# Kernel tuning notes

Measured on AMD Instinct MI355X. Metric: run time of the kernel, lower is better.

The kernel has to match this reference:

```python
import jax, jax.numpy as jnp
import numpy as np

B, C_IN, H, W = 64, 2048, 14, 14
D, FF, G, NC, NH = 768, 2048, 100, 9605, 8
DF = int(NC / G + 0.999)  # 97
HD = D // NH
EPS = 1e-5


def _ln(x, g, b):
    m = jnp.mean(x, axis=-1, keepdims=True)
    v = jnp.mean(jnp.square(x - m), axis=-1, keepdims=True)
    return (x - m) * jax.lax.rsqrt(v + EPS) * g + b


def setup_inputs() -> dict:
    key = jax.random.key(0)
    ks = jax.random.split(key, 16)
    def xav(k, shape):
        fan_in, fan_out = shape[-1], shape[-2] if len(shape) > 1 else shape[-1]
        std = float(np.sqrt(2.0 / (fan_in + fan_out)))
        return jax.random.normal(k, shape, jnp.float32) * std
    return {
        "x": jax.random.normal(ks[0], (B, C_IN, H, W), jnp.float32),
        "w_embed": xav(ks[1], (D, C_IN)), "b_embed": jnp.zeros((D,), jnp.float32),
        "query_embed": jax.random.normal(ks[2], (G, D), jnp.float32),
        "wq": xav(ks[3], (D, D)), "bq": jnp.zeros((D,), jnp.float32),
        "wk": xav(ks[4], (D, D)), "bk": jnp.zeros((D,), jnp.float32),
        "wv": xav(ks[5], (D, D)), "bv": jnp.zeros((D,), jnp.float32),
        "wo": xav(ks[6], (D, D)), "bo": jnp.zeros((D,), jnp.float32),
        "g1": jnp.ones((D,), jnp.float32), "be1": jnp.zeros((D,), jnp.float32),
        "g2": jnp.ones((D,), jnp.float32), "be2": jnp.zeros((D,), jnp.float32),
        "g3": jnp.ones((D,), jnp.float32), "be3": jnp.zeros((D,), jnp.float32),
        "w1": xav(ks[7], (FF, D)), "bl1": jnp.zeros((FF,), jnp.float32),
        "w2": xav(ks[8], (D, FF)), "bl2": jnp.zeros((D,), jnp.float32),
        "dup_pool": xav(ks[9], (G, D, DF)),
        "dup_bias": jnp.zeros((NC,), jnp.float32),
    }


def reference(x, w_embed, b_embed, query_embed, wq, bq, wk, bk, wv, bv, wo, bo,
              g1, be1, g2, be2, g3, be3, w1, bl1, w2, bl2, dup_pool, dup_bias):
    bs = x.shape[0]
    # [B, C, H, W] -> [B, S, C]
    mem = x.reshape(bs, x.shape[1], -1).transpose(0, 2, 1)
    # embed_standart + relu -> [B, S, D]
    mem = jax.nn.relu(jnp.einsum('bsc,dc->bsd', mem, w_embed) + b_embed)
    # tgt = queries broadcast to batch: [B, G, D]
    tgt = jnp.broadcast_to(query_embed[None], (bs, G, D))
    # layer: tgt = norm1(tgt + dropout1(tgt)) = norm1(2*tgt)
    tgt = _ln(tgt + tgt, g1, be1)
    # cross multihead attention (q=tgt, k=v=mem)
    q = (jnp.einsum('bgd,ed->bge', tgt, wq) + bq).reshape(bs, G, NH, HD)
    k = (jnp.einsum('bsd,ed->bse', mem, wk) + bk).reshape(bs, -1, NH, HD)
    v = (jnp.einsum('bsd,ed->bse', mem, wv) + bv).reshape(bs, -1, NH, HD)
    scores = jnp.einsum('bghd,bshd->bhgs', q, k) / jnp.sqrt(jnp.float32(HD))
    attn = jax.nn.softmax(scores, axis=-1)
    ctx = jnp.einsum('bhgs,bshd->bghd', attn, v).reshape(bs, G, D)
    ctx = jnp.einsum('bgd,ed->bge', ctx, wo) + bo
    tgt = _ln(tgt + ctx, g2, be2)
    # FFN
    ff = jax.nn.relu(jnp.einsum('bgd,fd->bgf', tgt, w1) + bl1)
    ff = jnp.einsum('bgf,df->bgd', ff, w2) + bl2
    h = _ln(tgt + ff, g3, be3)  # [B, G, D]
    # grouped FC: per-group matmul fused into one batched einsum
    out_extrap = jnp.einsum('bgd,gdf->bgf', h, dup_pool)  # [B, G, DF]
    logits = out_extrap.reshape(bs, G * DF)[:, :NC] + dup_bias
    return logits
```

## Files before the change

kernel.cpp:

```cpp
#include <hip/hip_runtime.h>
#include <hip/hip_bf16.h>


#define B_    64
#define CIN_  2048
#define S_    196
#define D_    768
#define FF_   2048
#define G_    100
#define NC_   9605
#define NH_   8
#define HD_   96
#define DF_   97
#define FP_   112
#define GP_   112
#define SP_   224
#define KVW_  1536
#define BS_   (B_ * S_)
#define BG_   (B_ * G_)

typedef __bf16 bf16x8 __attribute__((ext_vector_type(8)));
typedef float  f32x4  __attribute__((ext_vector_type(4)));

__device__ __forceinline__ float bf2f(ushort u) {
  union { unsigned int i; float f; } v; v.i = ((unsigned int)u) << 16; return v.f;
}
__device__ __forceinline__ ushort f2bf(float f) {
  __hip_bfloat16 h = __float2bfloat16(f);
  return *reinterpret_cast<ushort*>(&h);
}

__device__ __forceinline__ void gl2lds16(const ushort* g, ushort* l) {
  __builtin_amdgcn_global_load_lds((const __attribute__((address_space(1))) unsigned int*)g,
                                   (__attribute__((address_space(3))) unsigned int*)l, 16, 0, 0);
}

struct CvtArgs {
  const float* src[7];
  ushort*      dst[7];
  int          n4[7];
  int          total;
};
__global__ void k_cvtall(CvtArgs a) {
  int i = blockIdx.x * blockDim.x + threadIdx.x;
  const int stride = gridDim.x * blockDim.x;
  for (; i < a.total; i += stride) {
    int seg = 0, off = i;
    while (off >= a.n4[seg]) { off -= a.n4[seg]; ++seg; }
    float4 v = ((const float4*)a.src[seg])[off];
    ushort4 o;
    o.x = f2bf(v.x); o.y = f2bf(v.y); o.z = f2bf(v.z); o.w = f2bf(v.w);
    ((ushort4*)a.dst[seg])[off] = o;
  }
}

__global__ void k_packb(const float* __restrict__ bk, const float* __restrict__ bv,
                        float* __restrict__ bkv) {
  int i = blockIdx.x * 256 + threadIdx.x;
  if (i < D_) bkv[i] = bk[i];
  else if (i < 2 * D_) bkv[i] = bv[i - D_];
}

__global__ __launch_bounds__(256) void k_xpose(const float* __restrict__ x, ushort* __restrict__ A) {
  __shared__ float tile[32][33];
  const int c0 = blockIdx.x * 32, s0 = blockIdx.y * 32, b = blockIdx.z;
  const int t = threadIdx.x;
  const int tx = t & 31, ty = t >> 5;
  const float* xb = x + (size_t)b * CIN_ * S_;
  #pragma unroll
  for (int r = 0; r < 32; r += 8) {
    int c = c0 + ty + r, s = s0 + tx;
    tile[ty + r][tx] = (s < S_) ? xb[(size_t)c * S_ + s] : 0.f;
  }
  __syncthreads();
  const int sl = t >> 3, cq = (t & 7) * 4;
  const int s = s0 + sl;
  if (s < S_) {
    ushort4 o;
    o.x = f2bf(tile[cq + 0][sl]);
    o.y = f2bf(tile[cq + 1][sl]);
    o.z = f2bf(tile[cq + 2][sl]);
    o.w = f2bf(tile[cq + 3][sl]);
    *(ushort4*)&A[((size_t)(b * S_ + s)) * CIN_ + c0 + cq] = o;
  }
}

__global__ __launch_bounds__(256) void k_dupT(const float* __restrict__ dup, ushort* __restrict__ dupT) {
  __shared__ float tile[32][33];
  const int f0 = blockIdx.x * 32, d0 = blockIdx.y * 32, g = blockIdx.z;
  const int tx = threadIdx.x & 31, ty = threadIdx.x >> 5;
  #pragma unroll
  for (int r = 0; r < 32; r += 8) {
    int d = d0 + ty + r, f = f0 + tx;
    tile[ty + r][tx] = (f < DF_) ? dup[(size_t)g * D_ * DF_ + (size_t)d * DF_ + f] : 0.f;
  }
  __syncthreads();
  #pragma unroll
  for (int r = 0; r < 32; r += 8) {
    int f = f0 + ty + r, d = d0 + tx;
    if (f < FP_) dupT[((size_t)g * FP_ + f) * D_ + d] = f2bf(tile[tx][ty + r]);
  }
}

__global__ __launch_bounds__(256) void k_vT(const ushort* __restrict__ KVb, ushort* __restrict__ VbT) {
  __shared__ ushort tile[32][33];
  const int s0 = blockIdx.x * 32, d0 = blockIdx.y * 32, bh = blockIdx.z;
  const int b = bh >> 3, h = bh & 7;
  const int tx = threadIdx.x & 31, ty = threadIdx.x >> 5;
  #pragma unroll
  for (int r = 0; r < 32; r += 8) {
    int s = s0 + ty + r, d = d0 + tx;
    tile[ty + r][tx] = (s < S_) ? KVb[((size_t)(b * S_ + s)) * KVW_ + D_ + h * HD_ + d] : (ushort)0;
  }
  __syncthreads();
  #pragma unroll
  for (int r = 0; r < 32; r += 8) {
    int d = d0 + ty + r, s = s0 + tx;
    VbT[((size_t)bh * HD_ + d) * SP_ + s] = tile[tx][ty + r];
  }
}

__global__ __launch_bounds__(256) void k_tgt(const float* __restrict__ qe,
    const float* __restrict__ g1, const float* __restrict__ be1,
    float* __restrict__ tgt, ushort* __restrict__ tgtB) {
  const int g = blockIdx.x, t = threadIdx.x;
  if (g >= G_) {
    for (int d = t; d < D_; d += 256) tgtB[(size_t)g * D_ + d] = 0;
    return;
  }
  __shared__ float r1[256], r2[256];
  float y[3]; float s = 0.f, sq = 0.f;
  const float* row = qe + (size_t)g * D_;
  #pragma unroll
  for (int i = 0; i < 3; ++i) { float v = 2.f * row[t + i * 256]; y[i] = v; s += v; sq += v * v; }
  r1[t] = s; r2[t] = sq; __syncthreads();
  for (int o = 128; o > 0; o >>= 1) { if (t < o) { r1[t] += r1[t + o]; r2[t] += r2[t + o]; } __syncthreads(); }
  const float mean = r1[0] * (1.f / D_);
  const float var  = r2[0] * (1.f / D_) - mean * mean;
  const float w = rsqrtf(var + 1e-5f);
  #pragma unroll
  for (int i = 0; i < 3; ++i) {
    int d = t + i * 256;
    float v = (y[i] - mean) * w * g1[d] + be1[d];
    tgt[(size_t)g * D_ + d] = v;
    tgtB[(size_t)g * D_ + d] = f2bf(v);
  }
}

__global__ __launch_bounds__(256) void k_gemm(const ushort* __restrict__ A, const ushort* __restrict__ B,
    const float* __restrict__ bias, float* __restrict__ Cf, ushort* __restrict__ Cb,
    int N, int K, int nbx, int nm, int relu) {
  const int l = blockIdx.x;
  const int mb = (l >> 3) / nbx * 8 + (l & 7);
  const int nb = (l >> 3) % nbx;
  if (mb >= nm) return;
  __shared__ ushort As[128 * 32];
  __shared__ ushort Bs[128 * 32];
  const int t = threadIdx.x;
  const int m0 = mb * 128, n0 = nb * 128;
  const int lane = t & 63, wave = t >> 6;
  const int quad = lane >> 4, lrow = lane & 15;
  const int wr = (wave >> 1) * 64, wc = (wave & 1) * 64;
  const int srow = t >> 2, scol = (t & 3) * 8;
  f32x4 acc[4][4] = {};
  for (int k0 = 0; k0 < K; k0 += 32) {
    const ushort* ag = A + (size_t)(m0 + srow) * K + k0 + scol;
    const ushort* bg = B + (size_t)(n0 + srow) * K + k0 + scol;
    gl2lds16(ag,                    &As[srow * 32 + scol]);
    gl2lds16(ag + (size_t)64 * K,   &As[(srow + 64) * 32 + scol]);
    gl2lds16(bg,                    &Bs[srow * 32 + scol]);
    gl2lds16(bg + (size_t)64 * K,   &Bs[(srow + 64) * 32 + scol]);
    __syncthreads();
    bf16x8 af[4], bfr[4];
    #pragma unroll
    for (int i = 0; i < 4; ++i) af[i] = *(const bf16x8*)&As[(wr + i * 16 + lrow) * 32 + quad * 8];
    #pragma unroll
    for (int j = 0; j < 4; ++j) bfr[j] = *(const bf16x8*)&Bs[(wc + j * 16 + lrow) * 32 + quad * 8];
    #pragma unroll
    for (int i = 0; i < 4; ++i)
      #pragma unroll
      for (int j = 0; j < 4; ++j)
        acc[i][j] = __builtin_amdgcn_mfma_f32_16x16x32_bf16(af[i], bfr[j], acc[i][j], 0, 0, 0);
    __syncthreads();
  }
  #pragma unroll
  for (int i = 0; i < 4; ++i) {
    #pragma unroll
    for (int j = 0; j < 4; ++j) {
      const int gcol = n0 + wc + j * 16 + lrow;
      const float bv = bias ? bias[gcol] : 0.f;
      #pragma unroll
      for (int r = 0; r < 4; ++r) {
        const int grow = m0 + wr + i * 16 + quad * 4 + r;
        float v = acc[i][j][r] + bv;
        if (relu) v = fmaxf(v, 0.f);
        if (Cf) Cf[(size_t)grow * N + gcol] = v;
        else    Cb[(size_t)grow * N + gcol] = f2bf(v);
      }
    }
  }
}
static inline int swz_grid(int nm, int nbx) { return ((nm + 7) & ~7) * nbx; }

__global__ __launch_bounds__(256) void k_scores(const ushort* __restrict__ qB,
    const ushort* __restrict__ KVb, ushort* __restrict__ attnP) {
  __shared__ ushort Ks[208 * HD_];
  const int h = blockIdx.x, b = blockIdx.y, t = threadIdx.x;
  const int bh = b * NH_ + h;
  const int lane = t & 63, wave = t >> 6;
  const int quad = lane >> 4, c = lane & 15;
  for (int i = t; i < 208 * 12; i += 256) {
    int r = i / 12, col = (i % 12) * 8;
    gl2lds16(KVb + ((size_t)(b * S_ + r)) * KVW_ + h * HD_ + col, &Ks[i * 8]);
  }
  __syncthreads();
  const float scale = 0.1020620726f;
  for (int ii = wave; ii < 7; ii += 4) {
    f32x4 acc[13] = {};
    bf16x8 af[3];
    #pragma unroll
    for (int ks = 0; ks < 3; ++ks)
      af[ks] = *(const bf16x8*)(qB + ((size_t)(ii * 16 + c)) * D_ + h * HD_ + ks * 32 + quad * 8);
    #pragma unroll
    for (int j = 0; j < 13; ++j) {
      #pragma unroll
      for (int ks = 0; ks < 3; ++ks) {
        bf16x8 bf = *(const bf16x8*)&Ks[(j * 16 + c) * HD_ + ks * 32 + quad * 8];
        acc[j] = __builtin_amdgcn_mfma_f32_16x16x32_bf16(af[ks], bf, acc[j], 0, 0, 0);
      }
    }
    float m[4] = {-1e30f, -1e30f, -1e30f, -1e30f};
    #pragma unroll
    for (int j = 0; j < 13; ++j)
      #pragma unroll
      for (int r = 0; r < 4; ++r) {
        float v = acc[j][r] * scale;
        if (j == 12 && c >= 4) v = -1e30f;
        acc[j][r] = v;
        m[r] = fmaxf(m[r], v);
      }
    #pragma unroll
    for (int r = 0; r < 4; ++r) {
      m[r] = fmaxf(m[r], __shfl_xor(m[r], 1));
      m[r] = fmaxf(m[r], __shfl_xor(m[r], 2));
      m[r] = fmaxf(m[r], __shfl_xor(m[r], 4));
      m[r] = fmaxf(m[r], __shfl_xor(m[r], 8));
    }
    float l[4] = {0.f, 0.f, 0.f, 0.f};
    #pragma unroll
    for (int j = 0; j < 13; ++j)
      #pragma unroll
      for (int r = 0; r < 4; ++r) {
        float e = __expf(acc[j][r] - m[r]);
        acc[j][r] = e; l[r] += e;
      }
    #pragma unroll
    for (int r = 0; r < 4; ++r) {
      l[r] += __shfl_xor(l[r], 1);
      l[r] += __shfl_xor(l[r], 2);
      l[r] += __shfl_xor(l[r], 4);
      l[r] += __shfl_xor(l[r], 8);
      l[r] = 1.f / l[r];
    }
    #pragma unroll
    for (int j = 0; j < 13; ++j)
      #pragma unroll
      for (int r = 0; r < 4; ++r) {
        const int g = ii * 16 + quad * 4 + r;
        attnP[((size_t)bh * GP_ + g) * SP_ + j * 16 + c] = f2bf(acc[j][r] * l[r]);
      }
  }
}

__global__ __launch_bounds__(256) void k_pv(const ushort* __restrict__ attnP,
    const ushort* __restrict__ VbT, ushort* __restrict__ ctx) {
  __shared__ ushort Vs[HD_ * SP_];
  const int h = blockIdx.x, b = blockIdx.y, t = threadIdx.x;
  const int bh = b * NH_ + h;
  const int lane = t & 63, wave = t >> 6;
  const int quad = lane >> 4, c = lane & 15;
  const ushort* vsrc = VbT + (size_t)bh * HD_ * SP_;
  for (int i = t; i < HD_ * SP_ / 8; i += 256)
    gl2lds16(vsrc + (size_t)i * 8, &Vs[i * 8]);
  __syncthreads();
  for (int ii = wave; ii < 7; ii += 4) {
    bf16x8 af[7];
    #pragma unroll
    for (int k = 0; k < 7; ++k)
      af[k] = *(const bf16x8*)(attnP + ((size_t)bh * GP_ + ii * 16 + c) * SP_ + k * 32 + quad * 8);
    #pragma unroll
    for (int j = 0; j < 6; ++j) {
      f32x4 acc = {};
      #pragma unroll
      for (int k = 0; k < 7; ++k) {
        bf16x8 bf = *(const bf16x8*)&Vs[(j * 16 + c) * SP_ + k * 32 + quad * 8];
        acc = __builtin_amdgcn_mfma_f32_16x16x32_bf16(af[k], bf, acc, 0, 0, 0);
      }
      #pragma unroll
      for (int r = 0; r < 4; ++r) {
        const int g = ii * 16 + quad * 4 + r;
        if (g < G_)
          ctx[((size_t)(b * G_ + g)) * D_ + h * HD_ + j * 16 + c] = f2bf(acc[r]);
      }
    }
  }
}

__global__ __launch_bounds__(256) void k_lnres(const float* __restrict__ resid, int resid_mod,
    const float* __restrict__ add, const float* __restrict__ gamma, const float* __restrict__ beta,
    float* __restrict__ outf, ushort* __restrict__ outb, int transb) {
  const int row = blockIdx.x, t = threadIdx.x;
  __shared__ float r1[256], r2[256];
  const float* rrow = resid + (size_t)(resid_mod ? (row % G_) : row) * D_;
  const float* arow = add + (size_t)row * D_;
  float y[3]; float s = 0.f, sq = 0.f;
  #pragma unroll
  for (int i = 0; i < 3; ++i) {
    int d = t + i * 256;
    float v = rrow[d] + arow[d];
    y[i] = v; s += v; sq += v * v;
  }
  r1[t] = s; r2[t] = sq; __syncthreads();
  for (int o = 128; o > 0; o >>= 1) { if (t < o) { r1[t] += r1[t + o]; r2[t] += r2[t + o]; } __syncthreads(); }
  const float mean = r1[0] * (1.f / D_);
  const float var  = r2[0] * (1.f / D_) - mean * mean;
  const float w = rsqrtf(var + 1e-5f);
  const size_t orow = transb ? ((size_t)(row % G_) * B_ + row / G_) : (size_t)row;
  #pragma unroll
  for (int i = 0; i < 3; ++i) {
    int d = t + i * 256;
    float v = (y[i] - mean) * w * gamma[d] + beta[d];
    if (outf) outf[(size_t)row * D_ + d] = v;
    if (outb) outb[orow * D_ + d] = f2bf(v);
  }
}

__global__ __launch_bounds__(256) void k_head4(const ushort* __restrict__ hT,
    const ushort* __restrict__ dupT, const float* __restrict__ dup_bias, float* __restrict__ out) {
  const int g = blockIdx.x, j = blockIdx.y, t = threadIdx.x;
  const int lane = t & 63, wave = t >> 6;
  const int quad = lane >> 4, c = lane & 15;
  const ushort* ap = hT + ((size_t)g * B_ + wave * 16 + c) * D_;
  const ushort* bp = dupT + ((size_t)g * FP_ + j * 16 + c) * D_;
  f32x4 acc = {};
  #pragma unroll 8
  for (int k0 = 0; k0 < D_; k0 += 32) {
    bf16x8 af = *(const bf16x8*)(ap + k0 + quad * 8);
    bf16x8 bf = *(const bf16x8*)(bp + k0 + quad * 8);
    acc = __builtin_amdgcn_mfma_f32_16x16x32_bf16(af, bf, acc, 0, 0, 0);
  }
  const int f = j * 16 + c;
  if (f >= DF_) return;
  const int n = g * DF_ + f;
  if (n >= NC_) return;
  const float bv = dup_bias[n];
  #pragma unroll
  for (int r = 0; r < 4; ++r) {
    const int b = wave * 16 + quad * 4 + r;
    out[(size_t)b * NC_ + n] = acc[r] + bv;
  }
}

static constexpr size_t OFF_AEMB  = 0;
static constexpr size_t OFF_ATTNP = 0;
static constexpr size_t OFF_VBT   = 25690112;
static constexpr size_t OFF_FF    = 0;
static constexpr size_t OFF_FFO   = 26214400;
static constexpr size_t OFF_WEMB  = 51380224;
static constexpr size_t OFF_MEM   = 54525952;
static constexpr size_t OFF_WK    = 73793536;
static constexpr size_t OFF_WV    = 74973184;
static constexpr size_t OFF_WO    = 76152832;
static constexpr size_t OFF_W1    = 77332480;
static constexpr size_t OFF_W2    = 80478208;
static constexpr size_t OFF_DUP   = 83623936;
static constexpr size_t OFF_KV    = 100827136;
static constexpr size_t OFF_TGT   = 139362304;
static constexpr size_t OFF_TGTB  = 139669504;
static constexpr size_t OFF_Q     = 139866112;
static constexpr size_t OFF_BKV   = 140062720;
static constexpr size_t OFF_CTX   = 140068864;
static constexpr size_t OFF_WQ    = OFF_CTX;
static constexpr size_t OFF_CTXO  = 149899264;
static constexpr size_t OFF_TGT2F = 169560064;
static constexpr size_t OFF_TGT2B = 189220864;
static constexpr size_t OFF_HB    = 199051264;

extern "C" void kernel_launch(void* const* d_in, const int* in_sizes, int n_in,
                              void* d_out, int out_size, void* d_ws, size_t ws_size,
                              hipStream_t stream) {
  const float* x           = (const float*)d_in[0];
  const float* w_embed     = (const float*)d_in[1];
  const float* b_embed     = (const float*)d_in[2];
  const float* query_embed = (const float*)d_in[3];
  const float* wq          = (const float*)d_in[4];
  const float* bq          = (const float*)d_in[5];
  const float* wk          = (const float*)d_in[6];
  const float* bk          = (const float*)d_in[7];
  const float* wv          = (const float*)d_in[8];
  const float* bv          = (const float*)d_in[9];
  const float* wo          = (const float*)d_in[10];
  const float* bo          = (const float*)d_in[11];
  const float* g1          = (const float*)d_in[12];
  const float* be1         = (const float*)d_in[13];
  const float* g2          = (const float*)d_in[14];
  const float* be2         = (const float*)d_in[15];
  const float* g3          = (const float*)d_in[16];
  const float* be3         = (const float*)d_in[17];
  const float* w1          = (const float*)d_in[18];
  const float* bl1         = (const float*)d_in[19];
  const float* w2          = (const float*)d_in[20];
  const float* bl2         = (const float*)d_in[21];
  const float* dup_pool    = (const float*)d_in[22];
  const float* dup_bias    = (const float*)d_in[23];
  float* out = (float*)d_out;
  char* ws = (char*)d_ws;

  ushort* aemb  = (ushort*)(ws + OFF_AEMB);
  ushort* wembB = (ushort*)(ws + OFF_WEMB);
  ushort* memB  = (ushort*)(ws + OFF_MEM);
  ushort* wkvB  = (ushort*)(ws + OFF_WK);
  ushort* wkB   = (ushort*)(ws + OFF_WK);
  ushort* wvB   = (ushort*)(ws + OFF_WV);
  ushort* woB   = (ushort*)(ws + OFF_WO);
  ushort* w1B   = (ushort*)(ws + OFF_W1);
  ushort* w2B   = (ushort*)(ws + OFF_W2);
  ushort* wqB   = (ushort*)(ws + OFF_WQ);
  ushort* dupT  = (ushort*)(ws + OFF_DUP);
  ushort* KVb   = (ushort*)(ws + OFF_KV);
  float*  tgtF  = (float*)(ws + OFF_TGT);
  ushort* tgtB  = (ushort*)(ws + OFF_TGTB);
  ushort* qB    = (ushort*)(ws + OFF_Q);
  float*  bkvF  = (float*)(ws + OFF_BKV);
  ushort* attnP = (ushort*)(ws + OFF_ATTNP);
  ushort* VbT   = (ushort*)(ws + OFF_VBT);
  ushort* ctxB  = (ushort*)(ws + OFF_CTX);
  float*  ctxoF = (float*)(ws + OFF_CTXO);
  float*  tgt2F = (float*)(ws + OFF_TGT2F);
  ushort* tgt2B = (ushort*)(ws + OFF_TGT2B);
  ushort* ffB   = (ushort*)(ws + OFF_FF);
  float*  ffoF  = (float*)(ws + OFF_FFO);
  ushort* hT    = (ushort*)(ws + OFF_HB);

  CvtArgs ca;
  ca.src[0] = w_embed; ca.dst[0] = wembB; ca.n4[0] = D_ * CIN_ / 4;
  ca.src[1] = wk;      ca.dst[1] = wkB;   ca.n4[1] = D_ * D_ / 4;
  ca.src[2] = wv;      ca.dst[2] = wvB;   ca.n4[2] = D_ * D_ / 4;
  ca.src[3] = wo;      ca.dst[3] = woB;   ca.n4[3] = D_ * D_ / 4;
  ca.src[4] = w1;      ca.dst[4] = w1B;   ca.n4[4] = FF_ * D_ / 4;
  ca.src[5] = w2;      ca.dst[5] = w2B;   ca.n4[5] = D_ * FF_ / 4;
  ca.src[6] = wq;      ca.dst[6] = wqB;   ca.n4[6] = D_ * D_ / 4;
  ca.total = ca.n4[0] + ca.n4[1] + ca.n4[2] + ca.n4[3] + ca.n4[4] + ca.n4[5] + ca.n4[6];
  k_cvtall<<<2048, 256, 0, stream>>>(ca);
  k_packb<<<6, 256, 0, stream>>>(bk, bv, bkvF);
  k_dupT<<<dim3(4, 24, G_), 256, 0, stream>>>(dup_pool, dupT);

  k_xpose<<<dim3(CIN_ / 32, 7, B_), 256, 0, stream>>>(x, aemb);

  k_tgt<<<128, 256, 0, stream>>>(query_embed, g1, be1, tgtF, tgtB);

  k_gemm<<<swz_grid(1, 6), 256, 0, stream>>>(tgtB, wqB, bq, nullptr, qB, D_, D_, 6, 1, 0);

  k_gemm<<<swz_grid(98, 6), 256, 0, stream>>>(aemb, wembB, b_embed, nullptr, memB, D_, CIN_, 6, 98, 1);

  k_gemm<<<swz_grid(98, 12), 256, 0, stream>>>(memB, wkvB, bkvF, nullptr, KVb, KVW_, D_, 12, 98, 0);

  k_vT<<<dim3(7, 3, B_ * NH_), 256, 0, stream>>>(KVb, VbT);

  k_scores<<<dim3(NH_, B_), 256, 0, stream>>>(qB, KVb, attnP);
  k_pv<<<dim3(NH_, B_), 256, 0, stream>>>(attnP, VbT, ctxB);

  k_gemm<<<swz_grid(50, 6), 256, 0, stream>>>(ctxB, woB, bo, ctxoF, nullptr, D_, D_, 6, 50, 0);

  k_lnres<<<BG_, 256, 0, stream>>>(tgtF, 1, ctxoF, g2, be2, tgt2F, tgt2B, 0);

  k_gemm<<<swz_grid(50, 16), 256, 0, stream>>>(tgt2B, w1B, bl1, nullptr, ffB, FF_, D_, 16, 50, 1);
  k_gemm<<<swz_grid(50, 6), 256, 0, stream>>>(ffB, w2B, bl2, ffoF, nullptr, D_, FF_, 6, 50, 0);

  k_lnres<<<BG_, 256, 0, stream>>>(tgt2F, 0, ffoF, g3, be3, nullptr, hT, 1);

  k_head4<<<dim3(G_, 7), 256, 0, stream>>>(hT, dupT, dup_bias, out);
}
```

Measured before the change: 622.3 us.

## Fuse attention scores and PV, write V transposed from KV GEMM epilogue

Measured after the change: 612.3 us. About the same (-1.6%).

```diff
diff --git a/kernel.cpp b/kernel.cpp
--- a/kernel.cpp
+++ b/kernel.cpp
@@ -15,7 +15,6 @@
 #define FP_   112
 #define GP_   112
 #define SP_   224
-#define KVW_  1536
 #define BS_   (B_ * S_)
 #define BG_   (B_ * G_)
 
@@ -54,13 +53,6 @@
   }
 }
 
-__global__ void k_packb(const float* __restrict__ bk, const float* __restrict__ bv,
-                        float* __restrict__ bkv) {
-  int i = blockIdx.x * 256 + threadIdx.x;
-  if (i < D_) bkv[i] = bk[i];
-  else if (i < 2 * D_) bkv[i] = bv[i - D_];
-}
-
 __global__ __launch_bounds__(256) void k_xpose(const float* __restrict__ x, ushort* __restrict__ A) {
   __shared__ float tile[32][33];
   const int c0 = blockIdx.x * 32, s0 = blockIdx.y * 32, b = blockIdx.z;
@@ -102,24 +94,6 @@
   }
 }
 
-__global__ __launch_bounds__(256) void k_vT(const ushort* __restrict__ KVb, ushort* __restrict__ VbT) {
-  __shared__ ushort tile[32][33];
-  const int s0 = blockIdx.x * 32, d0 = blockIdx.y * 32, bh = blockIdx.z;
-  const int b = bh >> 3, h = bh & 7;
-  const int tx = threadIdx.x & 31, ty = threadIdx.x >> 5;
-  #pragma unroll
-  for (int r = 0; r < 32; r += 8) {
-    int s = s0 + ty + r, d = d0 + tx;
-    tile[ty + r][tx] = (s < S_) ? KVb[((size_t)(b * S_ + s)) * KVW_ + D_ + h * HD_ + d] : (ushort)0;
-  }
-  __syncthreads();
-  #pragma unroll
-  for (int r = 0; r < 32; r += 8) {
-    int d = d0 + ty + r, s = s0 + tx;
-    VbT[((size_t)bh * HD_ + d) * SP_ + s] = tile[tx][ty + r];
-  }
-}
-
 __global__ __launch_bounds__(256) void k_tgt(const float* __restrict__ qe,
     const float* __restrict__ g1, const float* __restrict__ be1,
     float* __restrict__ tgt, ushort* __restrict__ tgtB) {
@@ -148,7 +122,8 @@
 }
 
 __global__ __launch_bounds__(256) void k_gemm(const ushort* __restrict__ A, const ushort* __restrict__ B,
-    const float* __restrict__ bias, float* __restrict__ Cf, ushort* __restrict__ Cb,
+    const float* __restrict__ bias, const float* __restrict__ bias2,
+    float* __restrict__ Cf, ushort* __restrict__ Cb, ushort* __restrict__ Vt,
     int N, int K, int nbx, int nm, int relu) {
   const int l = blockIdx.x;
   const int mb = (l >> 3) / nbx * 8 + (l & 7);
@@ -188,55 +163,74 @@
     #pragma unroll
     for (int j = 0; j < 4; ++j) {
       const int gcol = n0 + wc + j * 16 + lrow;
-      const float bv = bias ? bias[gcol] : 0.f;
-      #pragma unroll
-      for (int r = 0; r < 4; ++r) {
-        const int grow = m0 + wr + i * 16 + quad * 4 + r;
-        float v = acc[i][j][r] + bv;
-        if (relu) v = fmaxf(v, 0.f);
-        if (Cf) Cf[(size_t)grow * N + gcol] = v;
-        else    Cb[(size_t)grow * N + gcol] = f2bf(v);
+      const float bv = (bias2 && gcol >= D_) ? bias2[gcol - D_] : (bias ? bias[gcol] : 0.f);
+      if (Vt && gcol >= D_) {
+        const int dv = gcol - D_, hh = dv / HD_, hd = dv % HD_;
+        const int row0 = m0 + wr + i * 16 + quad * 4;
+        const int bb = row0 / S_, ss = row0 % S_;
+        ushort4 o;
+        o.x = f2bf(acc[i][j][0] + bv);
+        o.y = f2bf(acc[i][j][1] + bv);
+        o.z = f2bf(acc[i][j][2] + bv);
+        o.w = f2bf(acc[i][j][3] + bv);
+        *(ushort4*)&Vt[((size_t)(bb * NH_ + hh) * HD_ + hd) * SP_ + ss] = o;
+      } else {
+        #pragma unroll
+        for (int r = 0; r < 4; ++r) {
+          const int grow = m0 + wr + i * 16 + quad * 4 + r;
+          float v = acc[i][j][r] + bv;
+          if (relu) v = fmaxf(v, 0.f);
+          if (Cf) Cf[(size_t)grow * N + gcol] = v;
+          else    Cb[(size_t)grow * N + gcol] = f2bf(v);
+        }
       }
     }
   }
 }
 static inline int swz_grid(int nm, int nbx) { return ((nm + 7) & ~7) * nbx; }
 
-__global__ __launch_bounds__(256) void k_scores(const ushort* __restrict__ qB,
-    const ushort* __restrict__ KVb, ushort* __restrict__ attnP) {
-  __shared__ ushort Ks[208 * HD_];
+__global__ __launch_bounds__(256) void k_attn(const ushort* __restrict__ qB,
+    const ushort* __restrict__ Kb, const ushort* __restrict__ VbT, ushort* __restrict__ ctx) {
+  __shared__ ushort lds[GP_ * SP_];
+  ushort* Ks = lds;
+  ushort* Ps = lds;
   const int h = blockIdx.x, b = blockIdx.y, t = threadIdx.x;
   const int bh = b * NH_ + h;
   const int lane = t & 63, wave = t >> 6;
   const int quad = lane >> 4, c = lane & 15;
   for (int i = t; i < 208 * 12; i += 256) {
     int r = i / 12, col = (i % 12) * 8;
-    gl2lds16(KVb + ((size_t)(b * S_ + r)) * KVW_ + h * HD_ + col, &Ks[i * 8]);
+    gl2lds16(Kb + ((size_t)(b * S_ + r)) * D_ + h * HD_ + col, &Ks[i * 8]);
   }
   __syncthreads();
   const float scale = 0.1020620726f;
-  for (int ii = wave; ii < 7; ii += 4) {
-    f32x4 acc[13] = {};
+  f32x4 p[2][13];
+  #pragma unroll
+  for (int rep = 0; rep < 2; ++rep) {
+    const int ii = wave + rep * 4;
+    if (ii >= 7) continue;
     bf16x8 af[3];
     #pragma unroll
     for (int ks = 0; ks < 3; ++ks)
       af[ks] = *(const bf16x8*)(qB + ((size_t)(ii * 16 + c)) * D_ + h * HD_ + ks * 32 + quad * 8);
     #pragma unroll
     for (int j = 0; j < 13; ++j) {
+      f32x4 a = {};
       #pragma unroll
       for (int ks = 0; ks < 3; ++ks) {
         bf16x8 bf = *(const bf16x8*)&Ks[(j * 16 + c) * HD_ + ks * 32 + quad * 8];
-        acc[j] = __builtin_amdgcn_mfma_f32_16x16x32_bf16(af[ks], bf, acc[j], 0, 0, 0);
-      }
+        a = __builtin_amdgcn_mfma_f32_16x16x32_bf16(af[ks], bf, a, 0, 0, 0);
+      }
+      p[rep][j] = a;
     }
     float m[4] = {-1e30f, -1e30f, -1e30f, -1e30f};
     #pragma unroll
     for (int j = 0; j < 13; ++j)
       #pragma unroll
       for (int r = 0; r < 4; ++r) {
-        float v = acc[j][r] * scale;
+        float v = p[rep][j][r] * scale;
         if (j == 12 && c >= 4) v = -1e30f;
-        acc[j][r] = v;
+        p[rep][j][r] = v;
         m[r] = fmaxf(m[r], v);
       }
     #pragma unroll
@@ -246,54 +240,57 @@
       m[r] = fmaxf(m[r], __shfl_xor(m[r], 4));
       m[r] = fmaxf(m[r], __shfl_xor(m[r], 8));
     }
-    float l[4] = {0.f, 0.f, 0.f, 0.f};
+    float lsum[4] = {0.f, 0.f, 0.f, 0.f};
     #pragma unroll
     for (int j = 0; j < 13; ++j)
       #pragma unroll
       for (int r = 0; r < 4; ++r) {
-        float e = __expf(acc[j][r] - m[r]);
-        acc[j][r] = e; l[r] += e;
+        float e = __expf(p[rep][j][r] - m[r]);
+        p[rep][j][r] = e; lsum[r] += e;
       }
     #pragma unroll
     for (int r = 0; r < 4; ++r) {
-      l[r] += __shfl_xor(l[r], 1);
-      l[r] += __shfl_xor(l[r], 2);
-      l[r] += __shfl_xor(l[r], 4);
-      l[r] += __shfl_xor(l[r], 8);
-      l[r] = 1.f / l[r];
+      lsum[r] += __shfl_xor(lsum[r], 1);
+      lsum[r] += __shfl_xor(lsum[r], 2);
+      lsum[r] += __shfl_xor(lsum[r], 4);
+      lsum[r] += __shfl_xor(lsum[r], 8);
+      lsum[r] = 1.f / lsum[r];
     }
     #pragma unroll
     for (int j = 0; j < 13; ++j)
       #pragma unroll
-      for (int r = 0; r < 4; ++r) {
-        const int g = ii * 16 + quad * 4 + r;
-        attnP[((size_t)bh * GP_ + g) * SP_ + j * 16 + c] = f2bf(acc[j][r] * l[r]);
-      }
-  }
-}
-
-__global__ __launch_bounds__(256) void k_pv(const ushort* __restrict__ attnP,
-    const ushort* __restrict__ VbT, ushort* __restrict__ ctx) {
-  __shared__ ushort Vs[HD_ * SP_];
-  const int h = blockIdx.x, b = blockIdx.y, t = threadIdx.x;
-  const int bh = b * NH_ + h;
-  const int lane = t & 63, wave = t >> 6;
-  const int quad = lane >> 4, c = lane & 15;
-  const ushort* vsrc = VbT + (size_t)bh * HD_ * SP_;
-  for (int i = t; i < HD_ * SP_ / 8; i += 256)
-    gl2lds16(vsrc + (size_t)i * 8, &Vs[i * 8]);
+      for (int r = 0; r < 4; ++r)
+        p[rep][j][r] *= lsum[r];
+  }
   __syncthreads();
-  for (int ii = wave; ii < 7; ii += 4) {
+  #pragma unroll
+  for (int rep = 0; rep < 2; ++rep) {
+    const int ii = wave + rep * 4;
+    if (ii >= 7) continue;
+    #pragma unroll
+    for (int r = 0; r < 4; ++r) {
+      const int g = ii * 16 + quad * 4 + r;
+      #pragma unroll
+      for (int j = 0; j < 13; ++j)
+        Ps[g * SP_ + j * 16 + c] = f2bf(p[rep][j][r]);
+      Ps[g * SP_ + 208 + c] = 0;
+    }
+  }
+  __syncthreads();
+  #pragma unroll
+  for (int rep = 0; rep < 2; ++rep) {
+    const int ii = wave + rep * 4;
+    if (ii >= 7) continue;
     bf16x8 af[7];
     #pragma unroll
     for (int k = 0; k < 7; ++k)
-      af[k] = *(const bf16x8*)(attnP + ((size_t)bh * GP_ + ii * 16 + c) * SP_ + k * 32 + quad * 8);
+      af[k] = *(const bf16x8*)&Ps[(ii * 16 + c) * SP_ + k * 32 + quad * 8];
     #pragma unroll
     for (int j = 0; j < 6; ++j) {
       f32x4 acc = {};
       #pragma unroll
       for (int k = 0; k < 7; ++k) {
-        bf16x8 bf = *(const bf16x8*)&Vs[(j * 16 + c) * SP_ + k * 32 + quad * 8];
+        bf16x8 bf = *(const bf16x8*)(VbT + ((size_t)bh * HD_ + j * 16 + c) * SP_ + k * 32 + quad * 8);
         acc = __builtin_amdgcn_mfma_f32_16x16x32_bf16(af[k], bf, acc, 0, 0, 0);
       }
       #pragma unroll
@@ -362,8 +359,7 @@
 }
 
 static constexpr size_t OFF_AEMB  = 0;
-static constexpr size_t OFF_ATTNP = 0;
-static constexpr size_t OFF_VBT   = 25690112;
+static constexpr size_t OFF_VBT   = 0;
 static constexpr size_t OFF_FF    = 0;
 static constexpr size_t OFF_FFO   = 26214400;
 static constexpr size_t OFF_WEMB  = 51380224;
@@ -374,11 +370,10 @@
 static constexpr size_t OFF_W1    = 77332480;
 static constexpr size_t OFF_W2    = 80478208;
 static constexpr size_t OFF_DUP   = 83623936;
-static constexpr size_t OFF_KV    = 100827136;
+static constexpr size_t OFF_KB    = 100827136;
 static constexpr size_t OFF_TGT   = 139362304;
 static constexpr size_t OFF_TGTB  = 139669504;
 static constexpr size_t OFF_Q     = 139866112;
-static constexpr size_t OFF_BKV   = 140062720;
 static constexpr size_t OFF_CTX   = 140068864;
 static constexpr size_t OFF_WQ    = OFF_CTX;
 static constexpr size_t OFF_CTXO  = 149899264;
@@ -427,12 +422,10 @@
   ushort* w2B   = (ushort*)(ws + OFF_W2);
   ushort* wqB   = (ushort*)(ws + OFF_WQ);
   ushort* dupT  = (ushort*)(ws + OFF_DUP);
-  ushort* KVb   = (ushort*)(ws + OFF_KV);
+  ushort* Kb    = (ushort*)(ws + OFF_KB);
   float*  tgtF  = (float*)(ws + OFF_TGT);
   ushort* tgtB  = (ushort*)(ws + OFF_TGTB);
   ushort* qB    = (ushort*)(ws + OFF_Q);
-  float*  bkvF  = (float*)(ws + OFF_BKV);
-  ushort* attnP = (ushort*)(ws + OFF_ATTNP);
   ushort* VbT   = (ushort*)(ws + OFF_VBT);
   ushort* ctxB  = (ushort*)(ws + OFF_CTX);
   float*  ctxoF = (float*)(ws + OFF_CTXO);
@@ -452,30 +445,32 @@
   ca.src[6] = wq;      ca.dst[6] = wqB;   ca.n4[6] = D_ * D_ / 4;
   ca.total = ca.n4[0] + ca.n4[1] + ca.n4[2] + ca.n4[3] + ca.n4[4] + ca.n4[5] + ca.n4[6];
   k_cvtall<<<2048, 256, 0, stream>>>(ca);
-  k_packb<<<6, 256, 0, stream>>>(bk, bv, bkvF);
   k_dupT<<<dim3(4, 24, G_), 256, 0, stream>>>(dup_pool, dupT);
 
   k_xpose<<<dim3(CIN_ / 32, 7, B_), 256, 0, stream>>>(x, aemb);
 
   k_tgt<<<128, 256, 0, stream>>>(query_embed, g1, be1, tgtF, tgtB);
 
-  k_gemm<<<swz_grid(1, 6), 256, 0, stream>>>(tgtB, wqB, bq, nullptr, qB, D_, D_, 6, 1, 0);
-
-  k_gemm<<<swz_grid(98, 6), 256, 0, stream>>>(aemb, wembB, b_embed, nullptr, memB, D_, CIN_, 6, 98, 1);
-
-  k_gemm<<<swz_grid(98, 12), 256, 0, stream>>>(memB, wkvB, bkvF, nullptr, KVb, KVW_, D_, 12, 98, 0);
-
-  k_vT<<<dim3(7, 3, B_ * NH_), 256, 0, stream>>>(KVb, VbT);
-
-  k_scores<<<dim3(NH_, B_), 256, 0, stream>>>(qB, KVb, attnP);
-  k_pv<<<dim3(NH_, B_), 256, 0, stream>>>(attnP, VbT, ctxB);
-
-  k_gemm<<<swz_grid(50, 6), 256, 0, stream>>>(ctxB, woB, bo, ctxoF, nullptr, D_, D_, 6, 50, 0);
+  k_gemm<<<swz_grid(1, 6), 256, 0, stream>>>(tgtB, wqB, bq, nullptr, nullptr, qB, nullptr,
+                                             D_, D_, 6, 1, 0);
+
+  k_gemm<<<swz_grid(98, 6), 256, 0, stream>>>(aemb, wembB, b_embed, nullptr, nullptr, memB, nullptr,
+                                              D_, CIN_, 6, 98, 1);
+
+  k_gemm<<<swz_grid(98, 12), 256, 0, stream>>>(memB, wkvB, bk, bv, nullptr, Kb, VbT,
+                                               D_, D_, 12, 98, 0);
+
+  k_attn<<<dim3(NH_, B_), 256, 0, stream>>>(qB, Kb, VbT, ctxB);
+
+  k_gemm<<<swz_grid(50, 6), 256, 0, stream>>>(ctxB, woB, bo, nullptr, ctxoF, nullptr, nullptr,
+                                              D_, D_, 6, 50, 0);
 
   k_lnres<<<BG_, 256, 0, stream>>>(tgtF, 1, ctxoF, g2, be2, tgt2F, tgt2B, 0);
 
-  k_gemm<<<swz_grid(50, 16), 256, 0, stream>>>(tgt2B, w1B, bl1, nullptr, ffB, FF_, D_, 16, 50, 1);
-  k_gemm<<<swz_grid(50, 6), 256, 0, stream>>>(ffB, w2B, bl2, ffoF, nullptr, D_, FF_, 6, 50, 0);
+  k_gemm<<<swz_grid(50, 16), 256, 0, stream>>>(tgt2B, w1B, bl1, nullptr, nullptr, ffB, nullptr,
+                                               FF_, D_, 16, 50, 1);
+  k_gemm<<<swz_grid(50, 6), 256, 0, stream>>>(ffB, w2B, bl2, nullptr, ffoF, nullptr, nullptr,
+                                              D_, FF_, 6, 50, 0);
 
   k_lnres<<<BG_, 256, 0, stream>>>(tgt2F, 0, ffoF, g3, be3, nullptr, hT, 1);
 
```
